# Performance work log

Measured on AMD Instinct MI355X. Metric: run time of the kernel, lower is better.

Reference implementation:

```python
import jax, jax.numpy as jnp
import numpy as np
import math

E = 512; H = 8; HD = E // H; FF = 2048; NLAYERS = 2
B = 128; QL = 32; DL = 512; K = 11
MU = jnp.array([1.0, 0.9, 0.7, 0.5, 0.3, 0.1, -0.1, -0.3, -0.5, -0.7, -0.9], dtype=jnp.float32)
SIGMA = jnp.array([0.001] + [0.1] * 10, dtype=jnp.float32)
BIN_PCT = 0.1; ABS_STEPS = 64; MAXLEN = 512
ABS_FACTORS = math.ceil(MAXLEN / ABS_STEPS)  # 8
POS_SELECTS = jnp.repeat(jnp.arange(1, ABS_FACTORS + 1), ABS_STEPS).astype(jnp.float32)  # [512]


def _sinusoid(dim, length):
    nts = dim // 2
    inc = math.log(10000.0) / (nts - 1)
    inv = np.exp(np.arange(nts) * -inc)
    sc = np.arange(length)[:, None] * inv[None, :]
    pe = np.concatenate([np.sin(sc), np.cos(sc)], axis=1)
    return jnp.asarray(pe[None], dtype=jnp.float32)  # [1, L, E]


def _ln(x, g, b):
    m = x.mean(-1, keepdims=True)
    v = ((x - m) ** 2).mean(-1, keepdims=True)
    return (x - m) / jnp.sqrt(v + 1e-5) * g + b


def _encoder(x, mask, iw, ib, ow, ob, f1w, f1b, f2w, f2b, g1, b1, g2, b2):
    # x: [B,S,E], mask: [B,S] float (1 = keep). PyTorch post-norm TransformerEncoderLayer, relu, dropout=0.
    bias = jnp.where(mask[:, None, None, :] > 0, 0.0, -1e9)  # key padding mask
    for l in range(iw.shape[0]):
        qkv = x @ iw[l].T + ib[l]
        q, k, v = jnp.split(qkv, 3, axis=-1)
        q = q.reshape(q.shape[0], q.shape[1], H, HD)
        k = k.reshape(k.shape[0], k.shape[1], H, HD)
        v = v.reshape(v.shape[0], v.shape[1], H, HD)
        s = jnp.einsum('bqhd,bkhd->bhqk', q, k) / math.sqrt(HD) + bias
        a = jax.nn.softmax(s, axis=-1)
        ctx = jnp.einsum('bhqk,bkhd->bqhd', a, v).reshape(x.shape)
        x = _ln(x + ctx @ ow[l].T + ob[l], g1[l], b1[l])
        h = jax.nn.relu(x @ f1w[l].T + f1b[l]) @ f2w[l].T + f2b[l]
        x = _ln(x + h, g2[l], b2[l])
    return x


def _forward(qe, de, qmask, dmask, pos_q, ln_g, ln_b, iw, ib, ow, ob, f1w, f1b, f2w, f2b,
             g1, b1, g2, b2, dense_w, pos_bias, pos_bias_abs):
    enc = lambda x, m: _encoder(x, m, iw, ib, ow, ob, f1w, f1b, f2w, f2b, g1, b1, g2, b2)
    q = enc(_ln(qe + pos_q[:, :qe.shape[1]], ln_g, ln_b), qmask)
    d = enc(_ln(de + pos_q[:, :de.shape[1]], ln_g, ln_b), dmask)
    qd_mask = qmask[:, :, None] * dmask[:, None, :]  # [B,Q,D]
    qn = q / (jnp.linalg.norm(q, axis=-1, keepdims=True) + 1e-13)
    dn = d / (jnp.linalg.norm(d, axis=-1, keepdims=True) + 1e-13)
    cos = jnp.einsum('bqe,bde->bqd', qn, dn) * qd_mask
    # RBF soft-histogram kernels: [B,Q,D,K]
    kr = jnp.exp(-(cos[..., None] - MU) ** 2 / (2.0 * SIGMA ** 2)) * qd_mask[..., None]
    # --- position bias ---
    doc_len = dmask.sum(1)  # [B]
    nbins = pos_bias.shape[0] - 1  # 10
    pos_range = (jnp.round(doc_len * BIN_PCT)[:, None] * jnp.arange(nbins, dtype=jnp.float32)).astype(jnp.int32)
    m = jnp.zeros_like(dmask).at[jnp.arange(dmask.shape[0])[:, None], pos_range].set(1.0)
    cs = jnp.cumsum(m, axis=1)
    pos_idx = (cs * dmask).astype(jnp.int32)  # [B,D] in [0, nbins]
    pbm = pos_bias[pos_idx][:, None, :, None]  # [B,1,D,1]
    abs_idx = (POS_SELECTS[:de.shape[1]] * dmask).astype(jnp.int32)
    abm = pos_bias_abs[abs_idx][:, None, :, None]  # [B,1,D,1]
    kr = kr * pbm * abm
    # --- kernel pooling ---
    per_kernel_query = kr.sum(2)  # [B,Q,K]
    logk = jnp.log(jnp.clip(per_kernel_query, 1e-10, None)) * qmask[:, :, None]
    per_kernel = logk.sum(1)  # [B,K]
    return (per_kernel @ dense_w.T)[:, 0]  # [B]


def setup_inputs() -> dict:
    key = jax.random.key(0)
    ks = jax.random.split(key, 8)
    s = 0.02
    return {
        'query_embeddings': jax.random.normal(ks[0], (B, QL, E), dtype=jnp.float32),
        'document_embeddings': jax.random.normal(ks[1], (B, DL, E), dtype=jnp.float32),
        'query_pad_oov_mask': jnp.ones((B, QL), dtype=jnp.float32),
        'document_pad_oov_mask': jnp.ones((B, DL), dtype=jnp.float32),
        'pos_q': _sinusoid(E, MAXLEN),
        'ln_g': jnp.ones((E,)), 'ln_b': jnp.zeros((E,)),
        'in_proj_w': jax.random.normal(ks[2], (NLAYERS, 3 * E, E)) * s,
        'in_proj_b': jnp.zeros((NLAYERS, 3 * E)),
        'out_w': jax.random.normal(ks[3], (NLAYERS, E, E)) * s,
        'out_b': jnp.zeros((NLAYERS, E)),
        'ff1_w': jax.random.normal(ks[4], (NLAYERS, FF, E)) * s,
        'ff1_b': jnp.zeros((NLAYERS, FF)),
        'ff2_w': jax.random.normal(ks[5], (NLAYERS, E, FF)) * s,
        'ff2_b': jnp.zeros((NLAYERS, E)),
        'n1_g': jnp.ones((NLAYERS, E)), 'n1_b': jnp.zeros((NLAYERS, E)),
        'n2_g': jnp.ones((NLAYERS, E)), 'n2_b': jnp.zeros((NLAYERS, E)),
        'dense_w': jax.random.normal(ks[6], (1, K)) * 0.1,
        'pos_bias': jnp.ones((int(1 / BIN_PCT) + 1,)).at[0].set(0.0),
        'pos_bias_abs': jnp.ones((ABS_FACTORS + 1,)).at[0].set(0.0),
    }


def reference(query_embeddings, document_embeddings, query_pad_oov_mask, document_pad_oov_mask,
              pos_q, ln_g, ln_b, in_proj_w, in_proj_b, out_w, out_b, ff1_w, ff1_b, ff2_w, ff2_b,
              n1_g, n1_b, n2_g, n2_b, dense_w, pos_bias, pos_bias_abs):
    return _forward(query_embeddings, document_embeddings, query_pad_oov_mask, document_pad_oov_mask,
                    pos_q, ln_g, ln_b, in_proj_w, in_proj_b, out_w, out_b, ff1_w, ff1_b, ff2_w, ff2_b,
                    n1_g, n1_b, n2_g, n2_b, dense_w, pos_bias, pos_bias_abs)
```

## Files before the change

### kernel.cpp

```cpp
#include <hip/hip_runtime.h>
#include <stdint.h>

typedef __bf16 bf16x8 __attribute__((ext_vector_type(8)));
typedef float f32x4 __attribute__((ext_vector_type(4)));
typedef unsigned short u16;
typedef unsigned int u32;

__device__ __forceinline__ u16 f2bf(float f) {
  u32 u = __float_as_uint(f);
  return (u16)((u + 0x7fffu + ((u >> 16) & 1u)) >> 16);
}

__device__ __forceinline__ void gload16(const void* g, void* l) {
  __builtin_amdgcn_global_load_lds((const __attribute__((address_space(1))) u32*)g,
                                   (__attribute__((address_space(3))) u32*)l, 16, 0, 0);
}

__device__ __forceinline__ f32x4 mfma16(bf16x8 a, bf16x8 b, f32x4 c) {
  return __builtin_amdgcn_mfma_f32_16x16x32_bf16(a, b, c, 0, 0, 0);
}

__global__ void cvt_k(const float* __restrict__ in, u16* __restrict__ out, int n4) {
  int i = blockIdx.x * blockDim.x + threadIdx.x;
  int stride = gridDim.x * blockDim.x;
  for (; i < n4; i += stride) {
    float4 v = ((const float4*)in)[i];
    ushort4 o;
    o.x = f2bf(v.x); o.y = f2bf(v.y); o.z = f2bf(v.z); o.w = f2bf(v.w);
    ((ushort4*)out)[i] = o;
  }
}

template<int MODE>
__global__ __launch_bounds__(128) void ln_k(const float* __restrict__ a, const float* __restrict__ bs,
                                            const float* __restrict__ g, const float* __restrict__ be,
                                            float* __restrict__ ox, u16* __restrict__ oxb, int S) {
  int row = blockIdx.x;
  int t = threadIdx.x;
  const float4* ar = (const float4*)(a + (size_t)row * 512);
  size_t brow = (MODE == 0) ? (size_t)(row % S) : (size_t)row;
  const float4* br = (const float4*)(bs + brow * 512);
  float4 va = ar[t], vb = br[t];
  float4 v;
  v.x = va.x + vb.x; v.y = va.y + vb.y; v.z = va.z + vb.z; v.w = va.w + vb.w;
  float s = v.x + v.y + v.z + v.w;
  float sq = v.x * v.x + v.y * v.y + v.z * v.z + v.w * v.w;
#pragma unroll
  for (int m = 1; m < 64; m <<= 1) { s += __shfl_xor(s, m); sq += __shfl_xor(sq, m); }
  __shared__ float red[2][2];
  int wv = t >> 6;
  if ((t & 63) == 0) { red[wv][0] = s; red[wv][1] = sq; }
  __syncthreads();
  s = red[0][0] + red[1][0];
  sq = red[0][1] + red[1][1];
  float mean = s * (1.f / 512.f);
  float var = sq * (1.f / 512.f) - mean * mean;
  float rstd = rsqrtf(var + 1e-5f);
  float4 vg = ((const float4*)g)[t], vbe = ((const float4*)be)[t];
  float4 y;
  y.x = (v.x - mean) * rstd * vg.x + vbe.x;
  y.y = (v.y - mean) * rstd * vg.y + vbe.y;
  y.z = (v.z - mean) * rstd * vg.z + vbe.z;
  y.w = (v.w - mean) * rstd * vg.w + vbe.w;
  ((float4*)(ox + (size_t)row * 512))[t] = y;
  ushort4 yb;
  yb.x = f2bf(y.x); yb.y = f2bf(y.y); yb.z = f2bf(y.z); yb.w = f2bf(y.w);
  ((ushort4*)(oxb + (size_t)row * 512))[t] = yb;
}

__global__ __launch_bounds__(128) void norm_k(const float* __restrict__ x, u16* __restrict__ o) {
  int row = blockIdx.x;
  int t = threadIdx.x;
  float4 v = ((const float4*)(x + (size_t)row * 512))[t];
  float sq = v.x * v.x + v.y * v.y + v.z * v.z + v.w * v.w;
#pragma unroll
  for (int m = 1; m < 64; m <<= 1) sq += __shfl_xor(sq, m);
  __shared__ float red[2];
  int wv = t >> 6;
  if ((t & 63) == 0) red[wv] = sq;
  __syncthreads();
  sq = red[0] + red[1];
  float rn = 1.f / (sqrtf(sq) + 1e-13f);
  ushort4 yb;
  yb.x = f2bf(v.x * rn); yb.y = f2bf(v.y * rn); yb.z = f2bf(v.z * rn); yb.w = f2bf(v.w * rn);
  ((ushort4*)(o + (size_t)row * 512))[t] = yb;
}

template<int OM>
__global__ __launch_bounds__(256) void gemm_bt(const u16* __restrict__ A, const u16* __restrict__ Bw,
                                               const float* __restrict__ bias, void* __restrict__ Cp,
                                               int M, int N, int Kd) {
  __shared__ __align__(16) u16 As[128 * 64];
  __shared__ __align__(16) u16 Bs[128 * 64];
  const int tid = threadIdx.x;
  const int w = tid >> 6, lane = tid & 63, lr = lane & 15, lg = lane >> 4;
  const int m0 = blockIdx.y * 128, n0 = blockIdx.x * 128;
  const int wr = w >> 1, wc = w & 1;
  f32x4 acc[4][4] = {};
  for (int k0 = 0; k0 < Kd; k0 += 64) {
    __syncthreads();
#pragma unroll
    for (int i = 0; i < 4; ++i) {
      int c = tid + 256 * i;
      int r = c >> 3, p = c & 7;
      int lc = p ^ (r & 7);
      gload16(A + (size_t)(m0 + r) * Kd + k0 + lc * 8, &As[c * 8]);
    }
#pragma unroll
    for (int i = 0; i < 4; ++i) {
      int c = tid + 256 * i;
      int r = c >> 3, p = c & 7;
      int lc = p ^ (r & 7);
      gload16(Bw + (size_t)(n0 + r) * Kd + k0 + lc * 8, &Bs[c * 8]);
    }
    __syncthreads();
#pragma unroll
    for (int ks = 0; ks < 2; ++ks) {
      bf16x8 af[4], bfr[4];
#pragma unroll
      for (int mi = 0; mi < 4; ++mi) {
        int m = wr * 64 + mi * 16 + lr;
        int ph = (ks * 4 + lg) ^ (m & 7);
        af[mi] = *(const bf16x8*)&As[m * 64 + ph * 8];
      }
#pragma unroll
      for (int ni = 0; ni < 4; ++ni) {
        int n = wc * 64 + ni * 16 + lr;
        int ph = (ks * 4 + lg) ^ (n & 7);
        bfr[ni] = *(const bf16x8*)&Bs[n * 64 + ph * 8];
      }
#pragma unroll
      for (int mi = 0; mi < 4; ++mi)
#pragma unroll
        for (int ni = 0; ni < 4; ++ni)
          acc[mi][ni] = mfma16(af[mi], bfr[ni], acc[mi][ni]);
    }
  }
#pragma unroll
  for (int ni = 0; ni < 4; ++ni) {
    int gn = n0 + wc * 64 + ni * 16 + lr;
    float bv = bias[gn];
#pragma unroll
    for (int mi = 0; mi < 4; ++mi) {
      int gmb = m0 + wr * 64 + mi * 16 + lg * 4;
#pragma unroll
      for (int r = 0; r < 4; ++r) {
        float v = acc[mi][ni][r] + bv;
        size_t off = (size_t)(gmb + r) * N + gn;
        if (OM == 0) {
          ((float*)Cp)[off] = v;
        } else {
          if (OM == 2) v = fmaxf(v, 0.f);
          ((u16*)Cp)[off] = f2bf(v);
        }
      }
    }
  }
}

__global__ __launch_bounds__(256) void attn_k(const u16* __restrict__ qkv, const float* __restrict__ mask,
                                              u16* __restrict__ ctx, int S, int nQ) {
  __shared__ __align__(16) u16 Kl[128 * 64];
  __shared__ __align__(16) u16 Vt[64 * 136];
  __shared__ __align__(16) u16 Pl[4][16 * 72];
  __shared__ float mb[128];
  const int tid = threadIdx.x, w = tid >> 6, lane = tid & 63, lr = lane & 15, lg = lane >> 4;
  const int bid = blockIdx.x;
  const int b = bid / (8 * nQ);
  const int rem = bid % (8 * nQ);
  const int h = rem / nQ, qb = rem % nQ;
  const int q0 = qb * 128;
  const size_t bbase = (size_t)b * S * 1536;

  bf16x8 aq[2][2];
  bool tv[2];
#pragma unroll
  for (int ti = 0; ti < 2; ++ti) {
    int row = q0 + w * 32 + ti * 16;
    tv[ti] = (row < S);
    if (tv[ti]) {
#pragma unroll
      for (int ks = 0; ks < 2; ++ks)
        aq[ti][ks] = *(const bf16x8*)(qkv + bbase + (size_t)(row + lr) * 1536 + h * 64 + ks * 32 + lg * 8);
    }
  }
  f32x4 o[2][4] = {};
  float mst[2][4], lst[2][4];
#pragma unroll
  for (int ti = 0; ti < 2; ++ti)
#pragma unroll
    for (int r = 0; r < 4; ++r) { mst[ti][r] = -1e30f; lst[ti][r] = 0.f; }

  const int nsc = (S + 127) / 128;
  for (int sc = 0; sc < nsc; ++sc) {
    int base = sc * 128;
    int vs = S - base; if (vs > 128) vs = 128;
    __syncthreads();
#pragma unroll
    for (int i = 0; i < 4; ++i) {
      int c = tid + 256 * i;
      int rr = c >> 3, p = c & 7;
      int lc = p ^ (rr & 7);
      bf16x8 val = {};
      if (rr < vs) val = *(const bf16x8*)(qkv + bbase + (size_t)(base + rr) * 1536 + 512 + h * 64 + lc * 8);
      *(bf16x8*)&Kl[rr * 64 + p * 8] = val;
    }
#pragma unroll
    for (int i = 0; i < 4; ++i) {
      int c = tid + 256 * i;
      int rr = c >> 3, p = c & 7;
      bf16x8 val = {};
      if (rr < vs) val = *(const bf16x8*)(qkv + bbase + (size_t)(base + rr) * 1536 + 1024 + h * 64 + p * 8);
#pragma unroll
      for (int j = 0; j < 8; ++j) Vt[(p * 8 + j) * 136 + rr] = ((const u16*)&val)[j];
    }
    if (tid < 128)
      mb[tid] = (tid < vs && mask[(size_t)b * S + base + tid] > 0.f) ? 0.f : -1e9f;
    __syncthreads();

    int nsub = (vs + 63) / 64;
#pragma unroll
    for (int ti = 0; ti < 2; ++ti) {
      if (!tv[ti]) continue;
      for (int sub = 0; sub < nsub; ++sub) {
        f32x4 sf[4] = {};
#pragma unroll
        for (int ks = 0; ks < 2; ++ks) {
#pragma unroll
          for (int ci = 0; ci < 4; ++ci) {
            int rr = sub * 64 + ci * 16 + lr;
            int ph = (ks * 4 + lg) ^ (rr & 7);
            bf16x8 kb = *(const bf16x8*)&Kl[rr * 64 + ph * 8];
            sf[ci] = mfma16(aq[ti][ks], kb, sf[ci]);
          }
        }
        float pv[4][4];
        float cm[4] = {-1e30f, -1e30f, -1e30f, -1e30f};
#pragma unroll
        for (int ci = 0; ci < 4; ++ci) {
          float bia = mb[sub * 64 + ci * 16 + lr];
#pragma unroll
          for (int r = 0; r < 4; ++r) {
            float v = sf[ci][r] * 0.125f + bia;
            pv[ci][r] = v;
            cm[r] = fmaxf(cm[r], v);
          }
        }
#pragma unroll
        for (int r = 0; r < 4; ++r) {
          float v = cm[r];
          v = fmaxf(v, __shfl_xor(v, 1));
          v = fmaxf(v, __shfl_xor(v, 2));
          v = fmaxf(v, __shfl_xor(v, 4));
          v = fmaxf(v, __shfl_xor(v, 8));
          cm[r] = v;
        }
        float al[4];
#pragma unroll
        for (int r = 0; r < 4; ++r) {
          float mn = fmaxf(mst[ti][r], cm[r]);
          al[r] = __expf(mst[ti][r] - mn);
          mst[ti][r] = mn;
        }
        float rs[4] = {0.f, 0.f, 0.f, 0.f};
#pragma unroll
        for (int ci = 0; ci < 4; ++ci)
#pragma unroll
          for (int r = 0; r < 4; ++r) {
            float p = __expf(pv[ci][r] - mst[ti][r]);
            pv[ci][r] = p;
            rs[r] += p;
          }
#pragma unroll
        for (int r = 0; r < 4; ++r) {
          float v = rs[r];
          v += __shfl_xor(v, 1); v += __shfl_xor(v, 2);
          v += __shfl_xor(v, 4); v += __shfl_xor(v, 8);
          lst[ti][r] = lst[ti][r] * al[r] + v;
        }
#pragma unroll
        for (int di = 0; di < 4; ++di)
#pragma unroll
          for (int r = 0; r < 4; ++r) o[ti][di][r] *= al[r];
#pragma unroll
        for (int ci = 0; ci < 4; ++ci)
#pragma unroll
          for (int r = 0; r < 4; ++r)
            Pl[w][(lg * 4 + r) * 72 + ci * 16 + lr] = f2bf(pv[ci][r]);
#pragma unroll
        for (int ks = 0; ks < 2; ++ks) {
          bf16x8 pa = *(const bf16x8*)&Pl[w][lr * 72 + ks * 32 + lg * 8];
#pragma unroll
          for (int di = 0; di < 4; ++di) {
            bf16x8 vb = *(const bf16x8*)&Vt[(di * 16 + lr) * 136 + sub * 64 + ks * 32 + lg * 8];
            o[ti][di] = mfma16(pa, vb, o[ti][di]);
          }
        }
      }
    }
  }
#pragma unroll
  for (int ti = 0; ti < 2; ++ti) {
    if (!tv[ti]) continue;
    int rowb = q0 + w * 32 + ti * 16 + lg * 4;
#pragma unroll
    for (int r = 0; r < 4; ++r) {
      float inv = 1.f / lst[ti][r];
#pragma unroll
      for (int di = 0; di < 4; ++di)
        ctx[(size_t)(b * S + rowb + r) * 512 + h * 64 + di * 16 + lr] = f2bf(o[ti][di][r] * inv);
    }
  }
}

__global__ __launch_bounds__(256) void cos_k(const u16* __restrict__ qn, const u16* __restrict__ dn,
                                             float* __restrict__ cosb) {
  int b = blockIdx.y;
  int n0 = blockIdx.x * 128;
  int tid = threadIdx.x, w = tid >> 6, lane = tid & 63, lr = lane & 15, lg = lane >> 4;
  const u16* qb_ = qn + (size_t)b * 32 * 512;
  const u16* db_ = dn + (size_t)b * 512 * 512;
  f32x4 acc[2][2] = {};
  for (int k0 = 0; k0 < 512; k0 += 32) {
    bf16x8 af[2], bfr[2];
#pragma unroll
    for (int mi = 0; mi < 2; ++mi)
      af[mi] = *(const bf16x8*)(qb_ + (size_t)(mi * 16 + lr) * 512 + k0 + lg * 8);
#pragma unroll
    for (int ni = 0; ni < 2; ++ni)
      bfr[ni] = *(const bf16x8*)(db_ + (size_t)(n0 + w * 32 + ni * 16 + lr) * 512 + k0 + lg * 8);
#pragma unroll
    for (int mi = 0; mi < 2; ++mi)
#pragma unroll
      for (int ni = 0; ni < 2; ++ni) acc[mi][ni] = mfma16(af[mi], bfr[ni], acc[mi][ni]);
  }
#pragma unroll
  for (int mi = 0; mi < 2; ++mi)
#pragma unroll
    for (int ni = 0; ni < 2; ++ni)
#pragma unroll
      for (int r = 0; r < 4; ++r)
        cosb[((size_t)b * 32 + mi * 16 + lg * 4 + r) * 512 + n0 + w * 32 + ni * 16 + lr] = acc[mi][ni][r];
}

__global__ __launch_bounds__(256) void pool_k(const float* __restrict__ cosb, const float* __restrict__ qm,
                                              const float* __restrict__ dm, const float* __restrict__ pb,
                                              const float* __restrict__ pba, const float* __restrict__ dw,
                                              float* __restrict__ out) {
  const float MUa[11] = {1.0f, 0.9f, 0.7f, 0.5f, 0.3f, 0.1f, -0.1f, -0.3f, -0.5f, -0.7f, -0.9f};
  const float INVa[11] = {500000.f, 50.f, 50.f, 50.f, 50.f, 50.f, 50.f, 50.f, 50.f, 50.f, 50.f};
  int b = blockIdx.x, tid = threadIdx.x, lane = tid & 63, wv = tid >> 6;
  __shared__ float wd[512];
  __shared__ float red[4][11];
  __shared__ float sred[4];
  float s = dm[(size_t)b * 512 + tid] + dm[(size_t)b * 512 + 256 + tid];
#pragma unroll
  for (int m = 1; m < 64; m <<= 1) s += __shfl_xor(s, m);
  if (lane == 0) sred[wv] = s;
  __syncthreads();
  float L = sred[0] + sred[1] + sred[2] + sred[3];
  int step = (int)rintf(L * 0.1f);
  for (int d = tid; d < 512; d += 256) {
    float mv = dm[(size_t)b * 512 + d];
    int cs = 1;
    if (step > 0) { cs = d / step + 1; if (cs > 10) cs = 10; }
    int pidx = (mv > 0.f) ? cs : 0;
    int aidx = (mv > 0.f) ? (1 + (d >> 6)) : 0;
    wd[d] = ((mv > 0.f) ? 1.f : 0.f) * pb[pidx] * pba[aidx];
  }
  float pk = 0.f;
  __syncthreads();
  for (int q = 0; q < 32; ++q) {
    float a[11] = {0.f, 0.f, 0.f, 0.f, 0.f, 0.f, 0.f, 0.f, 0.f, 0.f, 0.f};
    for (int d = tid; d < 512; d += 256) {
      float wdv = wd[d];
      if (wdv != 0.f) {
        float c = cosb[((size_t)b * 32 + q) * 512 + d];
#pragma unroll
        for (int k = 0; k < 11; ++k) {
          float t = c - MUa[k];
          a[k] += __expf(-t * t * INVa[k]) * wdv;
        }
      }
    }
#pragma unroll
    for (int k = 0; k < 11; ++k) {
      float v = a[k];
#pragma unroll
      for (int m = 1; m < 64; m <<= 1) v += __shfl_xor(v, m);
      a[k] = v;
    }
    if (lane == 0) {
#pragma unroll
      for (int k = 0; k < 11; ++k) red[wv][k] = a[k];
    }
    __syncthreads();
    if (tid < 11) {
      float sv = red[0][tid] + red[1][tid] + red[2][tid] + red[3][tid];
      pk += qm[(size_t)b * 32 + q] * logf(fmaxf(sv, 1e-10f));
    }
    __syncthreads();
  }
  if (tid < 11) red[0][tid] = pk * dw[tid];
  __syncthreads();
  if (tid == 0) {
    float t = 0.f;
#pragma unroll
    for (int k = 0; k < 11; ++k) t += red[0][k];
    out[b] = t;
  }
}

extern "C" void kernel_launch(void* const* d_in, const int* in_sizes, int n_in,
                              void* d_out, int out_size, void* d_ws, size_t ws_size,
                              hipStream_t stream) {
  (void)in_sizes; (void)n_in; (void)out_size;
  const float* qe  = (const float*)d_in[0];
  const float* de  = (const float*)d_in[1];
  const float* qm  = (const float*)d_in[2];
  const float* dmk = (const float*)d_in[3];
  const float* pos = (const float*)d_in[4];
  const float* lng = (const float*)d_in[5];
  const float* lnb = (const float*)d_in[6];
  const float* iw  = (const float*)d_in[7];
  const float* ib  = (const float*)d_in[8];
  const float* ow  = (const float*)d_in[9];
  const float* ob  = (const float*)d_in[10];
  const float* f1w = (const float*)d_in[11];
  const float* f1b = (const float*)d_in[12];
  const float* f2w = (const float*)d_in[13];
  const float* f2b = (const float*)d_in[14];
  const float* n1g = (const float*)d_in[15];
  const float* n1b = (const float*)d_in[16];
  const float* n2g = (const float*)d_in[17];
  const float* n2b = (const float*)d_in[18];
  const float* dw  = (const float*)d_in[19];
  const float* pb  = (const float*)d_in[20];
  const float* pba = (const float*)d_in[21];
  float* out = (float*)d_out;

  uint8_t* ws = (uint8_t*)d_ws;
  size_t off = 0;
  auto alloc = [&](size_t bytes) -> void* {
    void* p = ws + off;
    off += (bytes + 255) & ~(size_t)255;
    return p;
  };
  auto a256 = [](size_t b) -> size_t { return (b + 255) & ~(size_t)255; };

  u16* wb_iw = (u16*)alloc((size_t)2 * 1536 * 512 * 2);
  u16* wb_ow = (u16*)alloc((size_t)2 * 512 * 512 * 2);
  u16* wb_f1 = (u16*)alloc((size_t)2 * 2048 * 512 * 2);
  u16* wb_f2 = (u16*)alloc((size_t)2 * 512 * 2048 * 2);
  u16* qn_b  = (u16*)alloc((size_t)4096 * 512 * 2);
  u16* dn_b  = (u16*)alloc((size_t)65536 * 512 * 2);
  float* cosb = (float*)alloc((size_t)128 * 32 * 512 * 4);

  int cb = 128;
  while (cb > 8) {
    size_t rows = (size_t)cb * 512;
    size_t chunk = a256(rows * 512 * 4) + a256(rows * 512 * 2) +
                   a256(rows * 2048 * 2) + a256(rows * 512 * 4);
    if (off + chunk <= ws_size) break;
    cb >>= 1;
  }
  size_t rows_max = (size_t)cb * 512;
  float* x   = (float*)alloc(rows_max * 512 * 4);
  u16* xb    = (u16*)alloc(rows_max * 512 * 2);
  u16* big   = (u16*)alloc(rows_max * 2048 * 2);
  float* tmp = (float*)alloc(rows_max * 512 * 4);

  cvt_k<<<1024, 256, 0, stream>>>(iw,  wb_iw, 2 * 1536 * 512 / 4);
  cvt_k<<<1024, 256, 0, stream>>>(ow,  wb_ow, 2 * 512 * 512 / 4);
  cvt_k<<<1024, 256, 0, stream>>>(f1w, wb_f1, 2 * 2048 * 512 / 4);
  cvt_k<<<1024, 256, 0, stream>>>(f2w, wb_f2, 2 * 512 * 2048 / 4);

  auto enc = [&](const float* emb, const float* mask, int S, int nb) {
    int M = nb * S;
    u16* ctxb = big + (size_t)M * 1536;
    ln_k<0><<<M, 128, 0, stream>>>(emb, pos, lng, lnb, x, xb, S);
    int nQ = (S + 127) / 128;
    for (int l = 0; l < 2; ++l) {
      gemm_bt<1><<<dim3(12, M / 128), 256, 0, stream>>>(xb, wb_iw + (size_t)l * 1536 * 512,
                                                        ib + (size_t)l * 1536, big, M, 1536, 512);
      attn_k<<<nb * 8 * nQ, 256, 0, stream>>>(big, mask, ctxb, S, nQ);
      gemm_bt<0><<<dim3(4, M / 128), 256, 0, stream>>>(ctxb, wb_ow + (size_t)l * 512 * 512,
                                                       ob + (size_t)l * 512, tmp, M, 512, 512);
      ln_k<1><<<M, 128, 0, stream>>>(x, tmp, n1g + (size_t)l * 512, n1b + (size_t)l * 512, x, xb, S);
      gemm_bt<2><<<dim3(16, M / 128), 256, 0, stream>>>(xb, wb_f1 + (size_t)l * 2048 * 512,
                                                        f1b + (size_t)l * 2048, big, M, 2048, 512);
      gemm_bt<0><<<dim3(4, M / 128), 256, 0, stream>>>(big, wb_f2 + (size_t)l * 512 * 2048,
                                                       f2b + (size_t)l * 512, tmp, M, 512, 2048);
      ln_k<1><<<M, 128, 0, stream>>>(x, tmp, n2g + (size_t)l * 512, n2b + (size_t)l * 512, x, xb, S);
    }
  };

  for (int c0 = 0; c0 < 128; c0 += cb) {
    enc(de + (size_t)c0 * 512 * 512, dmk + (size_t)c0 * 512, 512, cb);
    norm_k<<<cb * 512, 128, 0, stream>>>(x, dn_b + (size_t)c0 * 512 * 512);
  }
  enc(qe, qm, 32, 128);
  norm_k<<<4096, 128, 0, stream>>>(x, qn_b);

  cos_k<<<dim3(4, 128), 256, 0, stream>>>(qn_b, dn_b, cosb);
  pool_k<<<128, 256, 0, stream>>>(cosb, qm, dmk, pb, pba, dw, out);
}
```

Baseline: 2.884 ms.

## Restructure attention kernel: async K loads, swizzled V transpose, shared K/V fragments

Full K tiles are now loaded with direct global-to-LDS transfers. The V transpose writes pairs of keys as 32-bit words into an XOR-swizzled layout to cut LDS bank conflicts. The loop order is swapped so the K and V register fragments are read once per 64-key subtile and reused for both query tiles, where before they were reloaded per tile. The MFMA sections are wrapped in s_setprio, and launch bounds now request 3 blocks per CU. The extra fragment registers could push up register pressure against the occupancy target.

```diff
diff --git a/kernel.cpp b/kernel.cpp
--- a/kernel.cpp
+++ b/kernel.cpp
@@ -158,8 +158,8 @@
   }
 }
 
-__global__ __launch_bounds__(256) void attn_k(const u16* __restrict__ qkv, const float* __restrict__ mask,
-                                              u16* __restrict__ ctx, int S, int nQ) {
+__global__ __launch_bounds__(256, 3) void attn_k(const u16* __restrict__ qkv, const float* __restrict__ mask,
+                                                 u16* __restrict__ ctx, int S, int nQ) {
   __shared__ __align__(16) u16 Kl[128 * 64];
   __shared__ __align__(16) u16 Vt[64 * 136];
   __shared__ __align__(16) u16 Pl[4][16 * 72];
@@ -196,56 +196,89 @@
     int base = sc * 128;
     int vs = S - base; if (vs > 128) vs = 128;
     __syncthreads();
-#pragma unroll
-    for (int i = 0; i < 4; ++i) {
+    if (vs == 128) {
+#pragma unroll
+      for (int i = 0; i < 4; ++i) {
+        int c = tid + 256 * i;
+        int r = c >> 3, p = c & 7;
+        int lc = p ^ (r & 7);
+        gload16(qkv + bbase + (size_t)(base + r) * 1536 + 512 + h * 64 + lc * 8, &Kl[c * 8]);
+      }
+    } else {
+#pragma unroll
+      for (int i = 0; i < 4; ++i) {
+        int c = tid + 256 * i;
+        int r = c >> 3, p = c & 7;
+        int lc = p ^ (r & 7);
+        bf16x8 val = {};
+        if (r < vs) val = *(const bf16x8*)(qkv + bbase + (size_t)(base + r) * 1536 + 512 + h * 64 + lc * 8);
+        *(bf16x8*)&Kl[c * 8] = val;
+      }
+    }
+#pragma unroll
+    for (int i = 0; i < 2; ++i) {
       int c = tid + 256 * i;
-      int rr = c >> 3, p = c & 7;
-      int lc = p ^ (rr & 7);
-      bf16x8 val = {};
-      if (rr < vs) val = *(const bf16x8*)(qkv + bbase + (size_t)(base + rr) * 1536 + 512 + h * 64 + lc * 8);
-      *(bf16x8*)&Kl[rr * 64 + p * 8] = val;
-    }
-#pragma unroll
-    for (int i = 0; i < 4; ++i) {
-      int c = tid + 256 * i;
-      int rr = c >> 3, p = c & 7;
-      bf16x8 val = {};
-      if (rr < vs) val = *(const bf16x8*)(qkv + bbase + (size_t)(base + rr) * 1536 + 1024 + h * 64 + p * 8);
-#pragma unroll
-      for (int j = 0; j < 8; ++j) Vt[(p * 8 + j) * 136 + rr] = ((const u16*)&val)[j];
+      int r2 = c >> 3, p = c & 7;
+      int k0 = 2 * r2;
+      bf16x8 v0 = {}, v1 = {};
+      if (k0 < vs)     v0 = *(const bf16x8*)(qkv + bbase + (size_t)(base + k0) * 1536 + 1024 + h * 64 + p * 8);
+      if (k0 + 1 < vs) v1 = *(const bf16x8*)(qkv + bbase + (size_t)(base + k0 + 1) * 1536 + 1024 + h * 64 + p * 8);
+      int pos = (((r2 >> 2) ^ p) << 3) + (k0 & 7);
+#pragma unroll
+      for (int j = 0; j < 8; ++j) {
+        u32 word = (u32)((const u16*)&v0)[j] | ((u32)((const u16*)&v1)[j] << 16);
+        *(u32*)&Vt[(p * 8 + j) * 136 + pos] = word;
+      }
     }
     if (tid < 128)
       mb[tid] = (tid < vs && mask[(size_t)b * S + base + tid] > 0.f) ? 0.f : -1e9f;
     __syncthreads();
 
     int nsub = (vs + 63) / 64;
-#pragma unroll
-    for (int ti = 0; ti < 2; ++ti) {
-      if (!tv[ti]) continue;
-      for (int sub = 0; sub < nsub; ++sub) {
+    for (int sub = 0; sub < nsub; ++sub) {
+      bf16x8 kb[2][4], vbf[2][4];
+      float bia[4];
+#pragma unroll
+      for (int ks = 0; ks < 2; ++ks)
+#pragma unroll
+        for (int ci = 0; ci < 4; ++ci) {
+          int rr = sub * 64 + ci * 16 + lr;
+          int ph = (ks * 4 + lg) ^ (rr & 7);
+          kb[ks][ci] = *(const bf16x8*)&Kl[rr * 64 + ph * 8];
+        }
+#pragma unroll
+      for (int ks = 0; ks < 2; ++ks)
+#pragma unroll
+        for (int di = 0; di < 4; ++di) {
+          int vrow = di * 16 + lr;
+          int g0 = sub * 8 + ks * 4 + lg;
+          int pos = ((g0 ^ ((vrow >> 3) & 7)) << 3);
+          vbf[ks][di] = *(const bf16x8*)&Vt[vrow * 136 + pos];
+        }
+#pragma unroll
+      for (int ci = 0; ci < 4; ++ci) bia[ci] = mb[sub * 64 + ci * 16 + lr];
+
+#pragma unroll
+      for (int ti = 0; ti < 2; ++ti) {
+        if (!tv[ti]) continue;
         f32x4 sf[4] = {};
-#pragma unroll
-        for (int ks = 0; ks < 2; ++ks) {
-#pragma unroll
-          for (int ci = 0; ci < 4; ++ci) {
-            int rr = sub * 64 + ci * 16 + lr;
-            int ph = (ks * 4 + lg) ^ (rr & 7);
-            bf16x8 kb = *(const bf16x8*)&Kl[rr * 64 + ph * 8];
-            sf[ci] = mfma16(aq[ti][ks], kb, sf[ci]);
-          }
-        }
+        __builtin_amdgcn_s_setprio(1);
+#pragma unroll
+        for (int ks = 0; ks < 2; ++ks)
+#pragma unroll
+          for (int ci = 0; ci < 4; ++ci)
+            sf[ci] = mfma16(aq[ti][ks], kb[ks][ci], sf[ci]);
+        __builtin_amdgcn_s_setprio(0);
         float pv[4][4];
         float cm[4] = {-1e30f, -1e30f, -1e30f, -1e30f};
 #pragma unroll
-        for (int ci = 0; ci < 4; ++ci) {
-          float bia = mb[sub * 64 + ci * 16 + lr];
+        for (int ci = 0; ci < 4; ++ci)
 #pragma unroll
           for (int r = 0; r < 4; ++r) {
-            float v = sf[ci][r] * 0.125f + bia;
+            float v = sf[ci][r] * 0.125f + bia[ci];
             pv[ci][r] = v;
             cm[r] = fmaxf(cm[r], v);
           }
-        }
 #pragma unroll
         for (int r = 0; r < 4; ++r) {
           float v = cm[r];
@@ -287,15 +320,15 @@
 #pragma unroll
           for (int r = 0; r < 4; ++r)
             Pl[w][(lg * 4 + r) * 72 + ci * 16 + lr] = f2bf(pv[ci][r]);
+        __builtin_amdgcn_s_setprio(1);
 #pragma unroll
         for (int ks = 0; ks < 2; ++ks) {
           bf16x8 pa = *(const bf16x8*)&Pl[w][lr * 72 + ks * 32 + lg * 8];
 #pragma unroll
-          for (int di = 0; di < 4; ++di) {
-            bf16x8 vb = *(const bf16x8*)&Vt[(di * 16 + lr) * 136 + sub * 64 + ks * 32 + lg * 8];
-            o[ti][di] = mfma16(pa, vb, o[ti][di]);
-          }
-        }
+          for (int di = 0; di < 4; ++di)
+            o[ti][di] = mfma16(pa, vbf[ks][di], o[ti][di]);
+        }
+        __builtin_amdgcn_s_setprio(0);
       }
     }
   }
```

After: 3.159 ms. +9.5%, slower.
